# Optimization experiments

Measured on AMD Instinct MI355X. Metric: run time of the kernel, lower is better.

The kernel has to match this reference:

```python
import jax, jax.numpy as jnp
import numpy as np

B, NC, H, W = 32, 4, 512, 512


def setup_inputs() -> dict:
    key = jax.random.key(0)
    k1, k2 = jax.random.split(key)
    predictions = jax.random.normal(k1, (B, NC, H, W), dtype=jnp.float32)
    targets = jax.random.uniform(k2, (B, NC, H, W), dtype=jnp.float32)
    return {"predictions": predictions, "targets": targets}


def reference(predictions, targets):
    # BCEWithLogitsLoss over flattened tensors (mean reduction), numerically stable
    ps = predictions
    ts = targets
    lseg = jnp.mean(jnp.maximum(ps, 0.0) - ps * ts + jnp.log1p(jnp.exp(-jnp.abs(ps))))

    nc = predictions.shape[1]
    preds = jnp.argmax(predictions, axis=1)  # [B, H, W] int
    tgt = jnp.argmax(targets, axis=1)        # [B, H, W] int

    cls = jnp.arange(nc)
    # one-hot masks [B, nc, H, W]
    pred_oh = (preds[:, None] == cls[None, :, None, None]).astype(jnp.float32)
    tgt_oh = (tgt[:, None] == cls[None, :, None, None]).astype(jnp.float32)

    # per-(batch, class) confusion counts in one pass (no host sync, no loop)
    TP = jnp.einsum('bchw,bchw->bc', tgt_oh, pred_oh)      # [B, nc]
    pred_cnt = pred_oh.sum(axis=(2, 3))                    # TP + FP
    tgt_cnt = tgt_oh.sum(axis=(2, 3))                      # TP + FN
    denom = pred_cnt + tgt_cnt - TP                        # TP + FP + FN

    iou_c = jnp.where(denom > 0, TP / denom, 0.0)          # nan_to_num(TP/denom)
    ious = iou_c.sum(axis=1)                               # [B]
    present = (tgt_cnt > 0).astype(jnp.float32).sum(axis=1)  # classes present per sample

    liou = 1.0 - jnp.mean(ious / present)
    return (lseg, liou)
```

## Files before the change

### kernel.cpp

```cpp
#include <hip/hip_runtime.h>


#define NB   32
#define NCL  4
constexpr int HW      = 512 * 512;
constexpr int GROUPS  = HW / 4;
constexpr int THREADS = 256;
constexpr int BLOCKS_PER_BATCH = 64;
constexpr int TPB = BLOCKS_PER_BATCH * THREADS;
constexpr int ITERS = GROUPS / TPB;

__global__ __launch_bounds__(THREADS, 8)
void seg_main(const float* __restrict__ pred,
              const float* __restrict__ tgt,
              float* __restrict__ bce_part,
              unsigned* __restrict__ pc_g,
              unsigned* __restrict__ tc_g,
              unsigned* __restrict__ tp_g)
{
    const int b     = blockIdx.x & (NB - 1);
    const int chunk = blockIdx.x >> 5;
    const int tib   = chunk * THREADS + threadIdx.x;

    const float* pp[NCL];
    const float* tq[NCL];
    {
        const size_t t0 = (size_t)b * NCL * HW + 4u * (size_t)tib;
#pragma unroll
        for (int c = 0; c < NCL; ++c) {
            pp[c] = pred + t0 + (size_t)c * HW;
            tq[c] = tgt  + t0 + (size_t)c * HW;
        }
    }

    float bce = 0.0f;
    unsigned pcP = 0u, tcP = 0u, tpP = 0u;

#pragma unroll
    for (int it = 0; it < ITERS; ++it) {
        const size_t soff = (size_t)it * 4u * TPB;
        float4 pv[NCL], tv[NCL];
#pragma unroll
        for (int c = 0; c < NCL; ++c) {
            pv[c] = *reinterpret_cast<const float4*>(pp[c] + soff);
            tv[c] = *reinterpret_cast<const float4*>(tq[c] + soff);
        }
#pragma unroll
        for (int j = 0; j < 4; ++j) {
            float pj[NCL], tj[NCL];
#pragma unroll
            for (int c = 0; c < NCL; ++c) {
                pj[c] = (&pv[c].x)[j];
                tj[c] = (&tv[c].x)[j];
            }
            int cp = 0, ct = 0;
            float bp = pj[0], bt = tj[0];
#pragma unroll
            for (int c = 1; c < NCL; ++c) {
                if (pj[c] > bp) { bp = pj[c]; cp = c; }
                if (tj[c] > bt) { bt = tj[c]; ct = c; }
            }
            const unsigned op = 1u << (cp << 3);
            const unsigned ot = 1u << (ct << 3);
            pcP += op;
            tcP += ot;
            tpP += (cp == ct) ? op : 0u;
#pragma unroll
            for (int c = 0; c < NCL; ++c) {
                const float p = pj[c];
                bce += fmaxf(p, 0.0f) - p * tj[c]
                     + __logf(1.0f + __expf(-fabsf(p)));
            }
        }
    }

    unsigned long long P = 0ull, T = 0ull, Q = 0ull;
#pragma unroll
    for (int c = 0; c < NCL; ++c) {
        P |= (unsigned long long)((pcP >> (8 * c)) & 0xFFu) << (16 * c);
        T |= (unsigned long long)((tcP >> (8 * c)) & 0xFFu) << (16 * c);
        Q |= (unsigned long long)((tpP >> (8 * c)) & 0xFFu) << (16 * c);
    }
#pragma unroll
    for (int o = 32; o > 0; o >>= 1) {
        bce += __shfl_xor(bce, o);
        P   += __shfl_xor(P, o);
        T   += __shfl_xor(T, o);
        Q   += __shfl_xor(Q, o);
    }

    __shared__ float              s_bce[THREADS / 64];
    __shared__ unsigned long long sP[THREADS / 64];
    __shared__ unsigned long long sT[THREADS / 64];
    __shared__ unsigned long long sQ[THREADS / 64];
    const int wid = threadIdx.x >> 6;
    if ((threadIdx.x & 63) == 0) {
        s_bce[wid] = bce; sP[wid] = P; sT[wid] = T; sQ[wid] = Q;
    }
    __syncthreads();
    if (threadIdx.x == 0) {
        float bs = s_bce[0] + s_bce[1] + s_bce[2] + s_bce[3];
        unsigned long long Ps = sP[0] + sP[1] + sP[2] + sP[3];
        unsigned long long Ts = sT[0] + sT[1] + sT[2] + sT[3];
        unsigned long long Qs = sQ[0] + sQ[1] + sQ[2] + sQ[3];
        atomicAdd(&bce_part[b], bs);
#pragma unroll
        for (int c = 0; c < NCL; ++c) {
            atomicAdd(&pc_g[b * NCL + c], (unsigned)((Ps >> (16 * c)) & 0xFFFFu));
            atomicAdd(&tc_g[b * NCL + c], (unsigned)((Ts >> (16 * c)) & 0xFFFFu));
            atomicAdd(&tp_g[b * NCL + c], (unsigned)((Qs >> (16 * c)) & 0xFFFFu));
        }
    }
}

__global__ void seg_final(const float* __restrict__ bce_part,
                          const unsigned* __restrict__ pc_g,
                          const unsigned* __restrict__ tc_g,
                          const unsigned* __restrict__ tp_g,
                          float* __restrict__ out)
{
    const int t = threadIdx.x;
    float val = 0.0f;
    float bs  = 0.0f;
    if (t < NB) {
        bs = bce_part[t];
        float iou = 0.0f;
        int present = 0;
#pragma unroll
        for (int c = 0; c < NCL; ++c) {
            const float P = (float)pc_g[t * NCL + c];
            const float T = (float)tc_g[t * NCL + c];
            const float K = (float)tp_g[t * NCL + c];
            const float den = P + T - K;
            if (den > 0.0f) iou += K / den;
            present += (tc_g[t * NCL + c] > 0u);
        }
        val = iou / (float)present;
    }
#pragma unroll
    for (int o = 32; o > 0; o >>= 1) {
        val += __shfl_xor(val, o);
        bs  += __shfl_xor(bs, o);
    }
    if (t == 0) {
        out[0] = bs / (float)((size_t)NB * NCL * HW);
        out[1] = 1.0f - val / (float)NB;
    }
}

extern "C" void kernel_launch(void* const* d_in, const int* in_sizes, int n_in,
                              void* d_out, int out_size, void* d_ws, size_t ws_size,
                              hipStream_t stream) {
    const float* pred = (const float*)d_in[0];
    const float* tgt  = (const float*)d_in[1];
    float* out = (float*)d_out;

    float*    bce_part = (float*)d_ws;
    unsigned* pc_g     = (unsigned*)((char*)d_ws + 256);
    unsigned* tc_g     = pc_g + NB * NCL;
    unsigned* tp_g     = tc_g + NB * NCL;

    hipMemsetAsync(d_ws, 0, 256 + 3 * NB * NCL * sizeof(unsigned), stream);
    seg_main<<<NB * BLOCKS_PER_BATCH, THREADS, 0, stream>>>(pred, tgt, bce_part,
                                                            pc_g, tc_g, tp_g);
    seg_final<<<1, 64, 0, stream>>>(bce_part, pc_g, tc_g, tp_g, out);
}
```

Measured before the change: 55.19 us.

## Fuse final reduction into main kernel via last-block counter and use native exp2/log

Merges the separate one-block finalize kernel into the main kernel: each block bumps a global counter after its atomics, and the last block computes the IoU and BCE outputs. This removes one kernel launch and its gap. It also swaps __expf/__logf for the raw amdgcn exp2/log builtins and applies the ln2 scale once per thread instead of once per element, which trims per-element ALU work. The cost is a threadfence plus a counter atomic per block, and a reliance on the fence pattern for correctness.

```diff
diff --git a/kernel.cpp b/kernel.cpp
--- a/kernel.cpp
+++ b/kernel.cpp
@@ -7,16 +7,19 @@
 constexpr int GROUPS  = HW / 4;
 constexpr int THREADS = 256;
 constexpr int BLOCKS_PER_BATCH = 64;
-constexpr int TPB = BLOCKS_PER_BATCH * THREADS;
-constexpr int ITERS = GROUPS / TPB;
+constexpr int NBLK    = NB * BLOCKS_PER_BATCH;
+constexpr int TPB     = BLOCKS_PER_BATCH * THREADS;
+constexpr int ITERS   = GROUPS / TPB;
 
 __global__ __launch_bounds__(THREADS, 8)
-void seg_main(const float* __restrict__ pred,
-              const float* __restrict__ tgt,
-              float* __restrict__ bce_part,
-              unsigned* __restrict__ pc_g,
-              unsigned* __restrict__ tc_g,
-              unsigned* __restrict__ tp_g)
+void seg_fused(const float* __restrict__ pred,
+               const float* __restrict__ tgt,
+               float* __restrict__ bce_part,
+               unsigned* __restrict__ counter,
+               unsigned* __restrict__ pc_g,
+               unsigned* __restrict__ tc_g,
+               unsigned* __restrict__ tp_g,
+               float* __restrict__ out)
 {
     const int b     = blockIdx.x & (NB - 1);
     const int chunk = blockIdx.x >> 5;
@@ -34,6 +37,7 @@
     }
 
     float bce = 0.0f;
+    float l2s = 0.0f;
     unsigned pcP = 0u, tcP = 0u, tpP = 0u;
 
 #pragma unroll
@@ -68,11 +72,14 @@
 #pragma unroll
             for (int c = 0; c < NCL; ++c) {
                 const float p = pj[c];
-                bce += fmaxf(p, 0.0f) - p * tj[c]
-                     + __logf(1.0f + __expf(-fabsf(p)));
+                bce += fmaxf(p, 0.0f) - p * tj[c];
+                l2s += __builtin_amdgcn_logf(
+                           1.0f + __builtin_amdgcn_exp2f(
+                                      fabsf(p) * -1.44269504f));
             }
         }
     }
+    bce += 0.69314718f * l2s;
 
     unsigned long long P = 0ull, T = 0ull, Q = 0ull;
 #pragma unroll
@@ -93,6 +100,7 @@
     __shared__ unsigned long long sP[THREADS / 64];
     __shared__ unsigned long long sT[THREADS / 64];
     __shared__ unsigned long long sQ[THREADS / 64];
+    __shared__ unsigned           s_old;
     const int wid = threadIdx.x >> 6;
     if ((threadIdx.x & 63) == 0) {
         s_bce[wid] = bce; sP[wid] = P; sT[wid] = T; sQ[wid] = Q;
@@ -110,15 +118,13 @@
             atomicAdd(&tc_g[b * NCL + c], (unsigned)((Ts >> (16 * c)) & 0xFFFFu));
             atomicAdd(&tp_g[b * NCL + c], (unsigned)((Qs >> (16 * c)) & 0xFFFFu));
         }
+        __threadfence();
+        s_old = atomicAdd(counter, 1u);
     }
-}
+    __syncthreads();
+    if (s_old != (unsigned)(NBLK - 1)) return;
 
-__global__ void seg_final(const float* __restrict__ bce_part,
-                          const unsigned* __restrict__ pc_g,
-                          const unsigned* __restrict__ tc_g,
-                          const unsigned* __restrict__ tp_g,
-                          float* __restrict__ out)
-{
+    __threadfence();
     const int t = threadIdx.x;
     float val = 0.0f;
     float bs  = 0.0f;
@@ -128,23 +134,25 @@
         int present = 0;
 #pragma unroll
         for (int c = 0; c < NCL; ++c) {
-            const float P = (float)pc_g[t * NCL + c];
-            const float T = (float)tc_g[t * NCL + c];
-            const float K = (float)tp_g[t * NCL + c];
-            const float den = P + T - K;
-            if (den > 0.0f) iou += K / den;
+            const float Pc = (float)pc_g[t * NCL + c];
+            const float Tc = (float)tc_g[t * NCL + c];
+            const float Kc = (float)tp_g[t * NCL + c];
+            const float den = Pc + Tc - Kc;
+            if (den > 0.0f) iou += Kc / den;
             present += (tc_g[t * NCL + c] > 0u);
         }
         val = iou / (float)present;
     }
+    if (t < 64) {
 #pragma unroll
-    for (int o = 32; o > 0; o >>= 1) {
-        val += __shfl_xor(val, o);
-        bs  += __shfl_xor(bs, o);
-    }
-    if (t == 0) {
-        out[0] = bs / (float)((size_t)NB * NCL * HW);
-        out[1] = 1.0f - val / (float)NB;
+        for (int o = 32; o > 0; o >>= 1) {
+            val += __shfl_xor(val, o);
+            bs  += __shfl_xor(bs, o);
+        }
+        if (t == 0) {
+            out[0] = bs / (float)((size_t)NB * NCL * HW);
+            out[1] = 1.0f - val / (float)NB;
+        }
     }
 }
 
@@ -156,12 +164,12 @@
     float* out = (float*)d_out;
 
     float*    bce_part = (float*)d_ws;
+    unsigned* counter  = (unsigned*)((char*)d_ws + 128);
     unsigned* pc_g     = (unsigned*)((char*)d_ws + 256);
     unsigned* tc_g     = pc_g + NB * NCL;
     unsigned* tp_g     = tc_g + NB * NCL;
 
     hipMemsetAsync(d_ws, 0, 256 + 3 * NB * NCL * sizeof(unsigned), stream);
-    seg_main<<<NB * BLOCKS_PER_BATCH, THREADS, 0, stream>>>(pred, tgt, bce_part,
-                                                            pc_g, tc_g, tp_g);
-    seg_final<<<1, 64, 0, stream>>>(bce_part, pc_g, tc_g, tp_g, out);
+    seg_fused<<<NBLK, THREADS, 0, stream>>>(pred, tgt, bce_part, counter,
+                                            pc_g, tc_g, tp_g, out);
 }
```

Measured after the change: 111.7 us. 2.02x slower.
